# Kernel optimization log

Measured on AMD Instinct MI355X. Metric: run time of the kernel, lower is better.

Reference implementation:

```python
import jax
import jax.numpy as jnp
import numpy as np
from jax import lax

B, T, D = 32, 256, 512   # batch, seq len, controller_dim (== memory_dim)
S = 2048                 # memory_slots
EPS_LN = 1e-5            # nn.LayerNorm default eps
EPS_NRM = 1e-12          # F.normalize default eps


def setup_inputs() -> dict:
    key = jax.random.key(0)
    ks = jax.random.split(key, 12)
    sc = 1.0 / np.sqrt(D)  # roughly torch Linear init scale
    return {
        "controller_seq": jax.random.normal(ks[0], (B, T, D), dtype=jnp.float32),
        "memory": jax.random.normal(ks[1], (S, D), dtype=jnp.float32),
        "Wk": jax.random.normal(ks[2], (D, D), dtype=jnp.float32) * sc,
        "bk": jax.random.normal(ks[3], (D,), dtype=jnp.float32) * sc,
        "We": jax.random.normal(ks[4], (D, D), dtype=jnp.float32) * sc,
        "be": jax.random.normal(ks[5], (D,), dtype=jnp.float32) * sc,
        "Ww": jax.random.normal(ks[6], (D, D), dtype=jnp.float32) * sc,
        "bw": jax.random.normal(ks[7], (D,), dtype=jnp.float32) * sc,
        "Wg": jax.random.normal(ks[8], (D, D), dtype=jnp.float32) * sc,
        "bg": jax.random.normal(ks[9], (D,), dtype=jnp.float32) * sc,
        "gamma": jnp.ones((D,), dtype=jnp.float32),
        "beta": jnp.zeros((D,), dtype=jnp.float32),
    }


def _l2norm(x, axis=-1):
    # matches F.normalize: x / max(||x||, eps)
    n = jnp.sqrt(jnp.sum(x * x, axis=axis, keepdims=True))
    return x / jnp.maximum(n, EPS_NRM)


def _layernorm(x, gamma, beta):
    mu = jnp.mean(x, axis=-1, keepdims=True)
    var = jnp.mean((x - mu) ** 2, axis=-1, keepdims=True)
    return (x - mu) * lax.rsqrt(var + EPS_LN) * gamma + beta


def reference(controller_seq, memory, Wk, bk, We, be, Ww, bw, Wg, bg, gamma, beta):
    batch = controller_seq.shape[0]

    def step(mem, c):  # mem: [S, Dm], c: [B, Dc]
        # --- read (addressing by cosine similarity) ---
        k = c @ Wk.T + bk                       # [B, Dm]
        sim = _l2norm(k) @ _l2norm(mem).T       # [B, S]
        w = jax.nn.softmax(sim, axis=-1)        # [B, S]
        read_val = w @ mem                      # [B, Dm]
        # --- write (erase / add, averaged over batch) ---
        erase = jax.nn.sigmoid(c @ We.T + be)   # [B, Dm]
        add = c @ Ww.T + bw                     # [B, Dm]
        # mean_b (1 - w_bs * e_bd) = 1 - (w^T e)/B ; avoids [B,S,Dm] intermediate
        erase_m = 1.0 - jnp.einsum("bs,bd->sd", w, erase) / batch
        add_m = jnp.einsum("bs,bd->sd", w, add) / batch
        new_mem = _layernorm(mem * erase_m + add_m, gamma, beta)  # dropout in eval mode
        # --- gated output ---
        g = jax.nn.sigmoid(c @ Wg.T + bg)       # [B, Dm]
        out_t = g * c + (1.0 - g) * read_val
        return new_mem, out_t

    _, outs = lax.scan(step, memory, jnp.swapaxes(controller_seq, 0, 1))  # outs: [T, B, D]
    return jnp.swapaxes(outs, 0, 1)  # [B, T, D]
```

## Files before the change

### kernel.cpp

```cpp
#include <hip/hip_runtime.h>

#define DEV __device__ __forceinline__

namespace {
constexpr int Bc = 32;
constexpr int Tc = 256;
constexpr int Dc = 512;
constexpr int Sc = 2048;
constexpr int NBLK = 256;
constexpr int NW   = 128;
constexpr int ROWS = Sc / NW;

constexpr size_t OFF_KN  = 0;
constexpr size_t OFF_E   = OFF_KN  + (size_t)Tc * Bc * Dc;
constexpr size_t OFF_A   = OFF_E   + (size_t)Tc * Bc * Dc;
constexpr size_t OFF_MEM = OFF_A   + (size_t)Tc * Bc * Dc;
constexpr size_t OFF_EW  = OFF_MEM + (size_t)2 * Sc * Dc;
constexpr size_t OFF_RP  = OFF_EW  + (size_t)2 * Sc * Bc;
constexpr size_t OFF_DEN = OFF_RP  + (size_t)2 * 16 * Bc * Dc;
}

DEV float sigm(float x) { return 1.0f / (1.0f + __expf(-x)); }

__global__ __launch_bounds__(256) void k_gemm(
    const float* __restrict__ A,
    const float* __restrict__ Wk, const float* __restrict__ bk,
    const float* __restrict__ We, const float* __restrict__ be,
    const float* __restrict__ Ww, const float* __restrict__ bw,
    const float* __restrict__ Wg, const float* __restrict__ bg,
    float* __restrict__ ws, float* __restrict__ gout)
{
  __shared__ float As[32][68];
  __shared__ float Bs[32][68];

  const int bid = blockIdx.x;
  const int mat = bid >> 10;
  const int rem = bid & 1023;
  const int rt = rem >> 3, jt = rem & 7;
  const int rbase = rt * 64, jbase = jt * 64;

  const float* Wm; const float* bm;
  if      (mat == 0) { Wm = Wk; bm = bk; }
  else if (mat == 1) { Wm = We; bm = be; }
  else if (mat == 2) { Wm = Ww; bm = bw; }
  else               { Wm = Wg; bm = bg; }

  const int tid = threadIdx.x;
  const int lr = tid >> 2;
  const int lk = (tid & 3) * 8;
  const int ty = tid >> 4, tx = tid & 15;

  float acc[4][4] = {};

  for (int k0 = 0; k0 < Dc; k0 += 32) {
    const float4 a0 = *(const float4*)&A [(size_t)(rbase + lr) * Dc + k0 + lk];
    const float4 a1 = *(const float4*)&A [(size_t)(rbase + lr) * Dc + k0 + lk + 4];
    const float4 b0 = *(const float4*)&Wm[(size_t)(jbase + lr) * Dc + k0 + lk];
    const float4 b1 = *(const float4*)&Wm[(size_t)(jbase + lr) * Dc + k0 + lk + 4];
    __syncthreads();
    As[lk + 0][lr] = a0.x; As[lk + 1][lr] = a0.y; As[lk + 2][lr] = a0.z; As[lk + 3][lr] = a0.w;
    As[lk + 4][lr] = a1.x; As[lk + 5][lr] = a1.y; As[lk + 6][lr] = a1.z; As[lk + 7][lr] = a1.w;
    Bs[lk + 0][lr] = b0.x; Bs[lk + 1][lr] = b0.y; Bs[lk + 2][lr] = b0.z; Bs[lk + 3][lr] = b0.w;
    Bs[lk + 4][lr] = b1.x; Bs[lk + 5][lr] = b1.y; Bs[lk + 6][lr] = b1.z; Bs[lk + 7][lr] = b1.w;
    __syncthreads();
    #pragma unroll
    for (int kk = 0; kk < 32; ++kk) {
      const float4 av = *(const float4*)&As[kk][ty * 4];
      const float4 bv = *(const float4*)&Bs[kk][tx * 4];
      const float ar[4] = {av.x, av.y, av.z, av.w};
      const float br[4] = {bv.x, bv.y, bv.z, bv.w};
      #pragma unroll
      for (int i = 0; i < 4; ++i)
        #pragma unroll
        for (int j = 0; j < 4; ++j)
          acc[i][j] = fmaf(ar[i], br[j], acc[i][j]);
    }
  }

  const float4 bias = *(const float4*)&bm[jbase + tx * 4];
  const float bi[4] = {bias.x, bias.y, bias.z, bias.w};
  #pragma unroll
  for (int i = 0; i < 4; ++i) {
    const int r = rbase + ty * 4 + i;
    float v[4];
    #pragma unroll
    for (int j = 0; j < 4; ++j) {
      v[j] = acc[i][j] + bi[j];
      if (mat & 1) v[j] = sigm(v[j]);
    }
    float4 o; o.x = v[0]; o.y = v[1]; o.z = v[2]; o.w = v[3];
    if (mat == 3) {
      *(float4*)&gout[(size_t)r * Dc + jbase + tx * 4] = o;
    } else {
      float* dst = ws + (mat == 0 ? OFF_KN : (mat == 1 ? OFF_E : OFF_A));
      const int t = r & 255, b = r >> 8;
      *(float4*)&dst[((size_t)t * Bc + b) * Dc + jbase + tx * 4] = o;
    }
  }
}

__global__ __launch_bounds__(256) void k_knorm(float* __restrict__ kn)
{
  const int row = blockIdx.x * 4 + (threadIdx.x >> 6);
  const int lane = threadIdx.x & 63;
  float* p = kn + (size_t)row * Dc;
  float4 v0 = *(const float4*)&p[lane * 4];
  float4 v1 = *(const float4*)&p[256 + lane * 4];
  float ss = v0.x*v0.x + v0.y*v0.y + v0.z*v0.z + v0.w*v0.w
           + v1.x*v1.x + v1.y*v1.y + v1.z*v1.z + v1.w*v1.w;
  #pragma unroll
  for (int off = 32; off >= 1; off >>= 1) ss += __shfl_xor(ss, off);
  const float inv = 1.0f / fmaxf(sqrtf(ss), 1e-12f);
  v0.x *= inv; v0.y *= inv; v0.z *= inv; v0.w *= inv;
  v1.x *= inv; v1.y *= inv; v1.z *= inv; v1.w *= inv;
  *(float4*)&p[lane * 4] = v0;
  *(float4*)&p[256 + lane * 4] = v1;
}

DEV void sim_phase(const float* __restrict__ knp, float* __restrict__ ewn,
                   float* __restrict__ denp, float (*xb)[516],
                   const float* invn_s, float* sred, int s0, int tid)
{
  const int r = tid >> 4, bp = tid & 15;
  const float* k0p = knp + (size_t)bp * Dc;
  const float* k1p = knp + (size_t)(bp + 16) * Dc;
  float acc0 = 0.f, acc1 = 0.f;
  #pragma unroll 4
  for (int dq = 0; dq < Dc / 4; ++dq) {
    const float4 y4 = *(const float4*)&xb[r][dq * 4];
    const float4 ka = *(const float4*)&k0p[dq * 4];
    const float4 kb = *(const float4*)&k1p[dq * 4];
    acc0 = fmaf(y4.x, ka.x, acc0); acc0 = fmaf(y4.y, ka.y, acc0);
    acc0 = fmaf(y4.z, ka.z, acc0); acc0 = fmaf(y4.w, ka.w, acc0);
    acc1 = fmaf(y4.x, kb.x, acc1); acc1 = fmaf(y4.y, kb.y, acc1);
    acc1 = fmaf(y4.z, kb.z, acc1); acc1 = fmaf(y4.w, kb.w, acc1);
  }
  const float iv = invn_s[r];
  const float e0 = __expf(acc0 * iv);
  const float e1 = __expf(acc1 * iv);
  ewn[(size_t)(s0 + r) * Bc + bp]      = e0;
  ewn[(size_t)(s0 + r) * Bc + bp + 16] = e1;
  if (tid < 32) sred[tid] = 0.f;
  __syncthreads();
  atomicAdd(&sred[bp], e0);
  atomicAdd(&sred[bp + 16], e1);
  __syncthreads();
  if (tid < 32) atomicAdd(&denp[tid], sred[tid]);
}

__global__ __launch_bounds__(256) void k_prologue(
    const float* __restrict__ mem_in, float* __restrict__ ws)
{
  __shared__ float xbuf[16][516];
  __shared__ float sred[32];
  __shared__ float invn_s[16];

  float* kn   = ws + OFF_KN;
  float* memb = ws + OFF_MEM;
  float* ewb  = ws + OFF_EW;
  float* den  = ws + OFF_DEN;

  const int bid = blockIdx.x, tid = threadIdx.x;
  const int s0 = bid * ROWS;
  const int c0 = tid * 2;
  #pragma unroll
  for (int r = 0; r < ROWS; ++r) {
    const float2 m = *(const float2*)&mem_in[(size_t)(s0 + r) * Dc + c0];
    *(float2*)&xbuf[r][c0] = m;
    *(float2*)&memb[(size_t)(s0 + r) * Dc + c0] = m;
  }
  __syncthreads();
  {
    const int row = tid >> 4, li = tid & 15;
    float ss = 0.f;
    #pragma unroll
    for (int i = 0; i < 8; ++i) {
      const float4 v = *(const float4*)&xbuf[row][(li + i * 16) * 4];
      ss += v.x*v.x + v.y*v.y + v.z*v.z + v.w*v.w;
    }
    ss += __shfl_xor(ss, 8); ss += __shfl_xor(ss, 4);
    ss += __shfl_xor(ss, 2); ss += __shfl_xor(ss, 1);
    if (li == 0) invn_s[row] = 1.0f / fmaxf(sqrtf(ss), 1e-12f);
  }
  __syncthreads();
  sim_phase(kn, ewb, den, xbuf, invn_s, sred, s0, tid);
}

__global__ __launch_bounds__(256) void k_step(
    int t,
    const float* __restrict__ cs,
    const float* __restrict__ gamma, const float* __restrict__ beta,
    float* __restrict__ ws, float* __restrict__ out)
{
  __shared__ float xbuf[16][516];
  __shared__ float wbuf[16][32];
  __shared__ float sred[32];
  __shared__ float mu_s[16], rs_s[16], invn_s[16];
  __shared__ float dinv_s[32];

  float* kn   = ws + OFF_KN;
  float* eptb = ws + OFF_E;
  float* aptb = ws + OFF_A;
  float* memb = ws + OFF_MEM;
  float* ewb  = ws + OFF_EW;
  float* rp   = ws + OFF_RP;
  float* den  = ws + OFF_DEN;

  const int bid = blockIdx.x, tid = threadIdx.x;
  const float inv32 = 1.0f / 32.0f;

  if (bid < NW) {
    if (t < Tc - 1) {
      const int s0 = bid * ROWS;
      const int c0 = tid * 2;
      const float* ewc = ewb + (size_t)(t & 1) * Sc * Bc;
      float*       ewn = ewb + (size_t)((t + 1) & 1) * Sc * Bc;
      const float* memc = memb + (size_t)(t & 1) * Sc * Dc;
      float*       memn = memb + (size_t)((t + 1) & 1) * Sc * Dc;

      if (tid < 32) dinv_s[tid] = 1.0f / den[(size_t)t * Bc + tid];
      __syncthreads();
      for (int idx = tid; idx < ROWS * 32; idx += 256) {
        const int r = idx >> 5, b = idx & 31;
        wbuf[r][b] = ewc[(size_t)(s0 + r) * Bc + b] * dinv_s[b];
      }
      __syncthreads();

      float2 er[ROWS] = {}, ad[ROWS] = {};
      const float* ept = eptb + (size_t)t * Bc * Dc;
      const float* apt = aptb + (size_t)t * Bc * Dc;
      #pragma unroll 4
      for (int b = 0; b < 32; ++b) {
        const float2 ev = *(const float2*)&ept[(size_t)b * Dc + c0];
        const float2 av = *(const float2*)&apt[(size_t)b * Dc + c0];
        #pragma unroll
        for (int r = 0; r < ROWS; ++r) {
          const float wv = wbuf[r][b];
          er[r].x = fmaf(wv, ev.x, er[r].x); er[r].y = fmaf(wv, ev.y, er[r].y);
          ad[r].x = fmaf(wv, av.x, ad[r].x); ad[r].y = fmaf(wv, av.y, ad[r].y);
        }
      }
      float2 xr[ROWS];
      #pragma unroll
      for (int r = 0; r < ROWS; ++r) {
        const float2 m = *(const float2*)&memc[(size_t)(s0 + r) * Dc + c0];
        float2 x;
        x.x = m.x * (1.0f - er[r].x * inv32) + ad[r].x * inv32;
        x.y = m.y * (1.0f - er[r].y * inv32) + ad[r].y * inv32;
        xr[r] = x;
        *(float2*)&xbuf[r][c0] = x;
      }
      __syncthreads();
      {
        const int row = tid >> 4, li = tid & 15;
        float s1 = 0.f, s2 = 0.f;
        #pragma unroll
        for (int i = 0; i < 8; ++i) {
          const float4 v = *(const float4*)&xbuf[row][(li + i * 16) * 4];
          s1 += v.x + v.y + v.z + v.w;
          s2 += v.x*v.x + v.y*v.y + v.z*v.z + v.w*v.w;
        }
        s1 += __shfl_xor(s1, 8); s2 += __shfl_xor(s2, 8);
        s1 += __shfl_xor(s1, 4); s2 += __shfl_xor(s2, 4);
        s1 += __shfl_xor(s1, 2); s2 += __shfl_xor(s2, 2);
        s1 += __shfl_xor(s1, 1); s2 += __shfl_xor(s2, 1);
        if (li == 0) {
          const float mu = s1 * (1.0f / 512.0f);
          const float var = s2 * (1.0f / 512.0f) - mu * mu;
          mu_s[row] = mu;
          rs_s[row] = rsqrtf(var + 1e-5f);
        }
      }
      __syncthreads();
      const float2 gm  = *(const float2*)&gamma[c0];
      const float2 bt2 = *(const float2*)&beta[c0];
      #pragma unroll
      for (int r = 0; r < ROWS; ++r) {
        const float mu = mu_s[r], rs = rs_s[r];
        float2 y;
        y.x = (xr[r].x - mu) * rs * gm.x + bt2.x;
        y.y = (xr[r].y - mu) * rs * gm.y + bt2.y;
        *(float2*)&xbuf[r][c0] = y;
        *(float2*)&memn[(size_t)(s0 + r) * Dc + c0] = y;
      }
      __syncthreads();
      {
        const int row = tid >> 4, li = tid & 15;
        float ss = 0.f;
        #pragma unroll
        for (int i = 0; i < 8; ++i) {
          const float4 v = *(const float4*)&xbuf[row][(li + i * 16) * 4];
          ss += v.x*v.x + v.y*v.y + v.z*v.z + v.w*v.w;
        }
        ss += __shfl_xor(ss, 8); ss += __shfl_xor(ss, 4);
        ss += __shfl_xor(ss, 2); ss += __shfl_xor(ss, 1);
        if (li == 0) invn_s[row] = 1.0f / fmaxf(sqrtf(ss), 1e-12f);
      }
      __syncthreads();
      sim_phase(kn + (size_t)(t + 1) * Bc * Dc, ewn,
                den + (size_t)(t + 1) * Bc, xbuf, invn_s, sred, s0, tid);
    }
  } else {
    const int rb = bid - NW;
    if (rb < 8 && t >= 1) {
      const int t0 = t - 1;
      const float* rpc = rp + (size_t)(t0 & 1) * 16 * Bc * Dc;
      const int base = (rb * 256 + tid) * 8;
      const int b = base >> 9, d0 = base & 511;
      const float inv = 1.0f / den[(size_t)t0 * Bc + b];
      float r0[4] = {}, r1[4] = {};
      #pragma unroll
      for (int si = 0; si < 16; ++si) {
        const float* q = rpc + ((size_t)si * Bc + b) * Dc + d0;
        const float4 p0 = *(const float4*)&q[0];
        const float4 p1 = *(const float4*)&q[4];
        r0[0] += p0.x; r0[1] += p0.y; r0[2] += p0.z; r0[3] += p0.w;
        r1[0] += p1.x; r1[1] += p1.y; r1[2] += p1.z; r1[3] += p1.w;
      }
      const size_t oofs = ((size_t)b * Tc + t0) * Dc + d0;
      const float4 g0 = *(const float4*)&out[oofs];
      const float4 g1 = *(const float4*)&out[oofs + 4];
      const float4 c0v = *(const float4*)&cs[oofs];
      const float4 c1v = *(const float4*)&cs[oofs + 4];
      float4 o0, o1;
      o0.x = g0.x * c0v.x + (1.0f - g0.x) * (r0[0] * inv);
      o0.y = g0.y * c0v.y + (1.0f - g0.y) * (r0[1] * inv);
      o0.z = g0.z * c0v.z + (1.0f - g0.z) * (r0[2] * inv);
      o0.w = g0.w * c0v.w + (1.0f - g0.w) * (r0[3] * inv);
      o1.x = g1.x * c1v.x + (1.0f - g1.x) * (r1[0] * inv);
      o1.y = g1.y * c1v.y + (1.0f - g1.y) * (r1[1] * inv);
      o1.z = g1.z * c1v.z + (1.0f - g1.z) * (r1[2] * inv);
      o1.w = g1.w * c1v.w + (1.0f - g1.w) * (r1[3] * inv);
      *(float4*)&out[oofs] = o0;
      *(float4*)&out[oofs + 4] = o1;
    }
    if (t < Tc) {
      const int si = rb >> 3, dj = rb & 7;
      const int sB = si * 128;
      const float* ewc = ewb + (size_t)(t & 1) * Sc * Bc;
      const float* memc = memb + (size_t)(t & 1) * Sc * Dc;
      float* ewl = (float*)xbuf;
      for (int i = tid; i < 128 * 32; i += 256) ewl[i] = ewc[(size_t)sB * Bc + i];
      __syncthreads();
      const int b = tid >> 3, dg = tid & 7;
      const int cbase = dj * 64 + dg * 8;
      float a0[4] = {}, a1[4] = {};
      #pragma unroll 2
      for (int s = 0; s < 128; ++s) {
        const float wv = ewl[s * 32 + b];
        const float* mrow = memc + (size_t)(sB + s) * Dc + cbase;
        const float4 m0 = *(const float4*)&mrow[0];
        const float4 m1 = *(const float4*)&mrow[4];
        a0[0] = fmaf(wv, m0.x, a0[0]); a0[1] = fmaf(wv, m0.y, a0[1]);
        a0[2] = fmaf(wv, m0.z, a0[2]); a0[3] = fmaf(wv, m0.w, a0[3]);
        a1[0] = fmaf(wv, m1.x, a1[0]); a1[1] = fmaf(wv, m1.y, a1[1]);
        a1[2] = fmaf(wv, m1.z, a1[2]); a1[3] = fmaf(wv, m1.w, a1[3]);
      }
      float* dst = rp + (size_t)(t & 1) * 16 * Bc * Dc + ((size_t)si * Bc + b) * Dc + cbase;
      float4 w0, w1;
      w0.x = a0[0]; w0.y = a0[1]; w0.z = a0[2]; w0.w = a0[3];
      w1.x = a1[0]; w1.y = a1[1]; w1.z = a1[2]; w1.w = a1[3];
      *(float4*)&dst[0] = w0;
      *(float4*)&dst[4] = w1;
    }
  }
}

extern "C" void kernel_launch(void* const* d_in, const int* in_sizes, int n_in,
                              void* d_out, int out_size, void* d_ws, size_t ws_size,
                              hipStream_t stream)
{
  const float* cs    = (const float*)d_in[0];
  const float* mem   = (const float*)d_in[1];
  const float* Wk    = (const float*)d_in[2];
  const float* bk    = (const float*)d_in[3];
  const float* We    = (const float*)d_in[4];
  const float* be    = (const float*)d_in[5];
  const float* Ww    = (const float*)d_in[6];
  const float* bw    = (const float*)d_in[7];
  const float* Wg    = (const float*)d_in[8];
  const float* bg    = (const float*)d_in[9];
  const float* gamma = (const float*)d_in[10];
  const float* beta  = (const float*)d_in[11];
  float* ws  = (float*)d_ws;
  float* out = (float*)d_out;

  hipMemsetAsync(ws + OFF_DEN, 0, (size_t)Tc * Bc * sizeof(float), stream);

  hipLaunchKernelGGL(k_gemm, dim3(4096), dim3(256), 0, stream,
                     cs, Wk, bk, We, be, Ww, bw, Wg, bg, ws, out);
  hipLaunchKernelGGL(k_knorm, dim3(2048), dim3(256), 0, stream, ws + OFF_KN);
  hipLaunchKernelGGL(k_prologue, dim3(NW), dim3(256), 0, stream, mem, ws);

  for (int t = 0; t <= Tc; ++t) {
    hipLaunchKernelGGL(k_step, dim3(NBLK), dim3(256), 0, stream,
                       t, cs, gamma, beta, ws, out);
  }
}
```

Before: 10.78 ms.

## Fuse per-step launches into one persistent kernel with grid barriers

Replaces the 257 per-timestep k_step launches with a single persistent k_main kernel that loops over time and synchronises all 256 blocks through an atomic-counter grid barrier. Cross-block data (memory, exp weights, denominators, partial reads) now goes through relaxed agent-scope atomic loads and stores so it stays visible across blocks inside one launch. This removes per-launch overhead and the kernel-boundary drain, at the cost of spin-waiting, narrower float2 accesses instead of float4, and reliance on all 256 blocks being resident at the same time.

```diff
diff --git a/kernel.cpp b/kernel.cpp
--- a/kernel.cpp
+++ b/kernel.cpp
@@ -18,9 +18,30 @@
 constexpr size_t OFF_EW  = OFF_MEM + (size_t)2 * Sc * Dc;
 constexpr size_t OFF_RP  = OFF_EW  + (size_t)2 * Sc * Bc;
 constexpr size_t OFF_DEN = OFF_RP  + (size_t)2 * 16 * Bc * Dc;
+constexpr size_t OFF_CNT = OFF_DEN + (size_t)Tc * Bc;
 }
 
 DEV float sigm(float x) { return 1.0f / (1.0f + __expf(-x)); }
+
+DEV float ld1cg(const float* p) {
+  unsigned u = __hip_atomic_load((const unsigned*)p, __ATOMIC_RELAXED,
+                                 __HIP_MEMORY_SCOPE_AGENT);
+  return __uint_as_float(u);
+}
+DEV void st1cg(float* p, float v) {
+  __hip_atomic_store((unsigned*)p, __float_as_uint(v), __ATOMIC_RELAXED,
+                     __HIP_MEMORY_SCOPE_AGENT);
+}
+DEV float2 ld2cg(const float* p) {
+  unsigned long long u = __hip_atomic_load((const unsigned long long*)p,
+                                           __ATOMIC_RELAXED, __HIP_MEMORY_SCOPE_AGENT);
+  union { unsigned long long u; float2 f; } c; c.u = u; return c.f;
+}
+DEV void st2cg(float* p, float2 v) {
+  union { float2 f; unsigned long long u; } c; c.f = v;
+  __hip_atomic_store((unsigned long long*)p, c.u, __ATOMIC_RELAXED,
+                     __HIP_MEMORY_SCOPE_AGENT);
+}
 
 __global__ __launch_bounds__(256) void k_gemm(
     const float* __restrict__ A,
@@ -138,8 +159,8 @@
   const float iv = invn_s[r];
   const float e0 = __expf(acc0 * iv);
   const float e1 = __expf(acc1 * iv);
-  ewn[(size_t)(s0 + r) * Bc + bp]      = e0;
-  ewn[(size_t)(s0 + r) * Bc + bp + 16] = e1;
+  st1cg(&ewn[(size_t)(s0 + r) * Bc + bp], e0);
+  st1cg(&ewn[(size_t)(s0 + r) * Bc + bp + 16], e1);
   if (tid < 32) sred[tid] = 0.f;
   __syncthreads();
   atomicAdd(&sred[bp], e0);
@@ -167,7 +188,7 @@
   for (int r = 0; r < ROWS; ++r) {
     const float2 m = *(const float2*)&mem_in[(size_t)(s0 + r) * Dc + c0];
     *(float2*)&xbuf[r][c0] = m;
-    *(float2*)&memb[(size_t)(s0 + r) * Dc + c0] = m;
+    st2cg(&memb[(size_t)(s0 + r) * Dc + c0], m);
   }
   __syncthreads();
   {
@@ -186,8 +207,21 @@
   sim_phase(kn, ewb, den, xbuf, invn_s, sred, s0, tid);
 }
 
-__global__ __launch_bounds__(256) void k_step(
-    int t,
+DEV void gbar(unsigned* cnt, unsigned target)
+{
+  __syncthreads();
+  if (threadIdx.x == 0) {
+    __hip_atomic_fetch_add(cnt, 1u, __ATOMIC_RELAXED, __HIP_MEMORY_SCOPE_AGENT);
+    unsigned v = __hip_atomic_load(cnt, __ATOMIC_RELAXED, __HIP_MEMORY_SCOPE_AGENT);
+    while (v < target) {
+      __builtin_amdgcn_s_sleep(2);
+      v = __hip_atomic_load(cnt, __ATOMIC_RELAXED, __HIP_MEMORY_SCOPE_AGENT);
+    }
+  }
+  __syncthreads();
+}
+
+__global__ __launch_bounds__(256) void k_main(
     const float* __restrict__ cs,
     const float* __restrict__ gamma, const float* __restrict__ beta,
     float* __restrict__ ws, float* __restrict__ out)
@@ -205,164 +239,174 @@
   float* ewb  = ws + OFF_EW;
   float* rp   = ws + OFF_RP;
   float* den  = ws + OFF_DEN;
+  unsigned* cnt = (unsigned*)(ws + OFF_CNT);
 
   const int bid = blockIdx.x, tid = threadIdx.x;
   const float inv32 = 1.0f / 32.0f;
-
-  if (bid < NW) {
-    if (t < Tc - 1) {
-      const int s0 = bid * ROWS;
-      const int c0 = tid * 2;
-      const float* ewc = ewb + (size_t)(t & 1) * Sc * Bc;
-      float*       ewn = ewb + (size_t)((t + 1) & 1) * Sc * Bc;
-      const float* memc = memb + (size_t)(t & 1) * Sc * Dc;
-      float*       memn = memb + (size_t)((t + 1) & 1) * Sc * Dc;
-
-      if (tid < 32) dinv_s[tid] = 1.0f / den[(size_t)t * Bc + tid];
-      __syncthreads();
-      for (int idx = tid; idx < ROWS * 32; idx += 256) {
-        const int r = idx >> 5, b = idx & 31;
-        wbuf[r][b] = ewc[(size_t)(s0 + r) * Bc + b] * dinv_s[b];
-      }
-      __syncthreads();
-
-      float2 er[ROWS] = {}, ad[ROWS] = {};
-      const float* ept = eptb + (size_t)t * Bc * Dc;
-      const float* apt = aptb + (size_t)t * Bc * Dc;
-      #pragma unroll 4
-      for (int b = 0; b < 32; ++b) {
-        const float2 ev = *(const float2*)&ept[(size_t)b * Dc + c0];
-        const float2 av = *(const float2*)&apt[(size_t)b * Dc + c0];
+  unsigned bart = 0;
+
+  for (int t = 0; t <= Tc; ++t) {
+    if (bid < NW) {
+      if (t < Tc - 1) {
+        const int s0 = bid * ROWS;
+        const int c0 = tid * 2;
+        const float* ewc = ewb + (size_t)(t & 1) * Sc * Bc;
+        float*       ewn = ewb + (size_t)((t + 1) & 1) * Sc * Bc;
+        const float* memc = memb + (size_t)(t & 1) * Sc * Dc;
+        float*       memn = memb + (size_t)((t + 1) & 1) * Sc * Dc;
+
+        if (tid < 32) dinv_s[tid] = 1.0f / ld1cg(&den[(size_t)t * Bc + tid]);
+        __syncthreads();
+        for (int idx = tid; idx < ROWS * 32; idx += 256) {
+          const int r = idx >> 5, b = idx & 31;
+          wbuf[r][b] = ld1cg(&ewc[(size_t)(s0 + r) * Bc + b]) * dinv_s[b];
+        }
+        __syncthreads();
+
+        float2 er[ROWS] = {}, ad[ROWS] = {};
+        const float* ept = eptb + (size_t)t * Bc * Dc;
+        const float* apt = aptb + (size_t)t * Bc * Dc;
+        #pragma unroll 4
+        for (int b = 0; b < 32; ++b) {
+          const float2 ev = *(const float2*)&ept[(size_t)b * Dc + c0];
+          const float2 av = *(const float2*)&apt[(size_t)b * Dc + c0];
+          #pragma unroll
+          for (int r = 0; r < ROWS; ++r) {
+            const float wv = wbuf[r][b];
+            er[r].x = fmaf(wv, ev.x, er[r].x); er[r].y = fmaf(wv, ev.y, er[r].y);
+            ad[r].x = fmaf(wv, av.x, ad[r].x); ad[r].y = fmaf(wv, av.y, ad[r].y);
+          }
+        }
+        float2 xr[ROWS];
         #pragma unroll
         for (int r = 0; r < ROWS; ++r) {
-          const float wv = wbuf[r][b];
-          er[r].x = fmaf(wv, ev.x, er[r].x); er[r].y = fmaf(wv, ev.y, er[r].y);
-          ad[r].x = fmaf(wv, av.x, ad[r].x); ad[r].y = fmaf(wv, av.y, ad[r].y);
-        }
+          const float2 m = ld2cg(&memc[(size_t)(s0 + r) * Dc + c0]);
+          float2 x;
+          x.x = m.x * (1.0f - er[r].x * inv32) + ad[r].x * inv32;
+          x.y = m.y * (1.0f - er[r].y * inv32) + ad[r].y * inv32;
+          xr[r] = x;
+          *(float2*)&xbuf[r][c0] = x;
+        }
+        __syncthreads();
+        {
+          const int row = tid >> 4, li = tid & 15;
+          float s1 = 0.f, s2 = 0.f;
+          #pragma unroll
+          for (int i = 0; i < 8; ++i) {
+            const float4 v = *(const float4*)&xbuf[row][(li + i * 16) * 4];
+            s1 += v.x + v.y + v.z + v.w;
+            s2 += v.x*v.x + v.y*v.y + v.z*v.z + v.w*v.w;
+          }
+          s1 += __shfl_xor(s1, 8); s2 += __shfl_xor(s2, 8);
+          s1 += __shfl_xor(s1, 4); s2 += __shfl_xor(s2, 4);
+          s1 += __shfl_xor(s1, 2); s2 += __shfl_xor(s2, 2);
+          s1 += __shfl_xor(s1, 1); s2 += __shfl_xor(s2, 1);
+          if (li == 0) {
+            const float mu = s1 * (1.0f / 512.0f);
+            const float var = s2 * (1.0f / 512.0f) - mu * mu;
+            mu_s[row] = mu;
+            rs_s[row] = rsqrtf(var + 1e-5f);
+          }
+        }
+        __syncthreads();
+        const float2 gm  = *(const float2*)&gamma[c0];
+        const float2 bt2 = *(const float2*)&beta[c0];
+        #pragma unroll
+        for (int r = 0; r < ROWS; ++r) {
+          const float mu = mu_s[r], rs = rs_s[r];
+          float2 y;
+          y.x = (xr[r].x - mu) * rs * gm.x + bt2.x;
+          y.y = (xr[r].y - mu) * rs * gm.y + bt2.y;
+          *(float2*)&xbuf[r][c0] = y;
+          st2cg(&memn[(size_t)(s0 + r) * Dc + c0], y);
+        }
+        __syncthreads();
+        {
+          const int row = tid >> 4, li = tid & 15;
+          float ss = 0.f;
+          #pragma unroll
+          for (int i = 0; i < 8; ++i) {
+            const float4 v = *(const float4*)&xbuf[row][(li + i * 16) * 4];
+            ss += v.x*v.x + v.y*v.y + v.z*v.z + v.w*v.w;
+          }
+          ss += __shfl_xor(ss, 8); ss += __shfl_xor(ss, 4);
+          ss += __shfl_xor(ss, 2); ss += __shfl_xor(ss, 1);
+          if (li == 0) invn_s[row] = 1.0f / fmaxf(sqrtf(ss), 1e-12f);
+        }
+        __syncthreads();
+        sim_phase(kn + (size_t)(t + 1) * Bc * Dc, ewn,
+                  den + (size_t)(t + 1) * Bc, xbuf, invn_s, sred, s0, tid);
       }
-      float2 xr[ROWS];
-      #pragma unroll
-      for (int r = 0; r < ROWS; ++r) {
-        const float2 m = *(const float2*)&memc[(size_t)(s0 + r) * Dc + c0];
-        float2 x;
-        x.x = m.x * (1.0f - er[r].x * inv32) + ad[r].x * inv32;
-        x.y = m.y * (1.0f - er[r].y * inv32) + ad[r].y * inv32;
-        xr[r] = x;
-        *(float2*)&xbuf[r][c0] = x;
+    } else {
+      const int rb = bid - NW;
+      if (rb < 8 && t >= 1) {
+        const int t0 = t - 1;
+        const float* rpc = rp + (size_t)(t0 & 1) * 16 * Bc * Dc;
+        const int base = (rb * 256 + tid) * 8;
+        const int b = base >> 9, d0 = base & 511;
+        const float inv = 1.0f / ld1cg(&den[(size_t)t0 * Bc + b]);
+        float r0[8] = {};
+        #pragma unroll
+        for (int si = 0; si < 16; ++si) {
+          const float* q = rpc + ((size_t)si * Bc + b) * Dc + d0;
+          const float2 p0 = ld2cg(q + 0);
+          const float2 p1 = ld2cg(q + 2);
+          const float2 p2 = ld2cg(q + 4);
+          const float2 p3 = ld2cg(q + 6);
+          r0[0] += p0.x; r0[1] += p0.y; r0[2] += p1.x; r0[3] += p1.y;
+          r0[4] += p2.x; r0[5] += p2.y; r0[6] += p3.x; r0[7] += p3.y;
+        }
+        const size_t oofs = ((size_t)b * Tc + t0) * Dc + d0;
+        const float4 g0 = *(const float4*)&out[oofs];
+        const float4 g1 = *(const float4*)&out[oofs + 4];
+        const float4 c0v = *(const float4*)&cs[oofs];
+        const float4 c1v = *(const float4*)&cs[oofs + 4];
+        float4 o0, o1;
+        o0.x = g0.x * c0v.x + (1.0f - g0.x) * (r0[0] * inv);
+        o0.y = g0.y * c0v.y + (1.0f - g0.y) * (r0[1] * inv);
+        o0.z = g0.z * c0v.z + (1.0f - g0.z) * (r0[2] * inv);
+        o0.w = g0.w * c0v.w + (1.0f - g0.w) * (r0[3] * inv);
+        o1.x = g1.x * c1v.x + (1.0f - g1.x) * (r0[4] * inv);
+        o1.y = g1.y * c1v.y + (1.0f - g1.y) * (r0[5] * inv);
+        o1.z = g1.z * c1v.z + (1.0f - g1.z) * (r0[6] * inv);
+        o1.w = g1.w * c1v.w + (1.0f - g1.w) * (r0[7] * inv);
+        *(float4*)&out[oofs] = o0;
+        *(float4*)&out[oofs + 4] = o1;
       }
-      __syncthreads();
-      {
-        const int row = tid >> 4, li = tid & 15;
-        float s1 = 0.f, s2 = 0.f;
-        #pragma unroll
-        for (int i = 0; i < 8; ++i) {
-          const float4 v = *(const float4*)&xbuf[row][(li + i * 16) * 4];
-          s1 += v.x + v.y + v.z + v.w;
-          s2 += v.x*v.x + v.y*v.y + v.z*v.z + v.w*v.w;
-        }
-        s1 += __shfl_xor(s1, 8); s2 += __shfl_xor(s2, 8);
-        s1 += __shfl_xor(s1, 4); s2 += __shfl_xor(s2, 4);
-        s1 += __shfl_xor(s1, 2); s2 += __shfl_xor(s2, 2);
-        s1 += __shfl_xor(s1, 1); s2 += __shfl_xor(s2, 1);
-        if (li == 0) {
-          const float mu = s1 * (1.0f / 512.0f);
-          const float var = s2 * (1.0f / 512.0f) - mu * mu;
-          mu_s[row] = mu;
-          rs_s[row] = rsqrtf(var + 1e-5f);
-        }
+      if (t < Tc) {
+        const int si = rb >> 3, dj = rb & 7;
+        const int sB = si * 128;
+        const float* ewc = ewb + (size_t)(t & 1) * Sc * Bc;
+        const float* memc = memb + (size_t)(t & 1) * Sc * Dc;
+        float* ewl = (float*)xbuf;
+        for (int i = tid; i < 128 * 32; i += 256)
+          ewl[i] = ld1cg(&ewc[(size_t)sB * Bc + i]);
+        __syncthreads();
+        const int b = tid >> 3, dg = tid & 7;
+        const int cbase = dj * 64 + dg * 8;
+        float a0[8] = {};
+        #pragma unroll 2
+        for (int s = 0; s < 128; ++s) {
+          const float wv = ewl[s * 32 + b];
+          const float* mrow = memc + (size_t)(sB + s) * Dc + cbase;
+          const float2 m0 = ld2cg(mrow + 0);
+          const float2 m1 = ld2cg(mrow + 2);
+          const float2 m2 = ld2cg(mrow + 4);
+          const float2 m3 = ld2cg(mrow + 6);
+          a0[0] = fmaf(wv, m0.x, a0[0]); a0[1] = fmaf(wv, m0.y, a0[1]);
+          a0[2] = fmaf(wv, m1.x, a0[2]); a0[3] = fmaf(wv, m1.y, a0[3]);
+          a0[4] = fmaf(wv, m2.x, a0[4]); a0[5] = fmaf(wv, m2.y, a0[5]);
+          a0[6] = fmaf(wv, m3.x, a0[6]); a0[7] = fmaf(wv, m3.y, a0[7]);
+        }
+        float* dst = rp + (size_t)(t & 1) * 16 * Bc * Dc + ((size_t)si * Bc + b) * Dc + cbase;
+        float2 w0; w0.x = a0[0]; w0.y = a0[1]; st2cg(dst + 0, w0);
+        float2 w1; w1.x = a0[2]; w1.y = a0[3]; st2cg(dst + 2, w1);
+        float2 w2; w2.x = a0[4]; w2.y = a0[5]; st2cg(dst + 4, w2);
+        float2 w3; w3.x = a0[6]; w3.y = a0[7]; st2cg(dst + 6, w3);
+        __syncthreads();
       }
-      __syncthreads();
-      const float2 gm  = *(const float2*)&gamma[c0];
-      const float2 bt2 = *(const float2*)&beta[c0];
-      #pragma unroll
-      for (int r = 0; r < ROWS; ++r) {
-        const float mu = mu_s[r], rs = rs_s[r];
-        float2 y;
-        y.x = (xr[r].x - mu) * rs * gm.x + bt2.x;
-        y.y = (xr[r].y - mu) * rs * gm.y + bt2.y;
-        *(float2*)&xbuf[r][c0] = y;
-        *(float2*)&memn[(size_t)(s0 + r) * Dc + c0] = y;
-      }
-      __syncthreads();
-      {
-        const int row = tid >> 4, li = tid & 15;
-        float ss = 0.f;
-        #pragma unroll
-        for (int i = 0; i < 8; ++i) {
-          const float4 v = *(const float4*)&xbuf[row][(li + i * 16) * 4];
-          ss += v.x*v.x + v.y*v.y + v.z*v.z + v.w*v.w;
-        }
-        ss += __shfl_xor(ss, 8); ss += __shfl_xor(ss, 4);
-        ss += __shfl_xor(ss, 2); ss += __shfl_xor(ss, 1);
-        if (li == 0) invn_s[row] = 1.0f / fmaxf(sqrtf(ss), 1e-12f);
-      }
-      __syncthreads();
-      sim_phase(kn + (size_t)(t + 1) * Bc * Dc, ewn,
-                den + (size_t)(t + 1) * Bc, xbuf, invn_s, sred, s0, tid);
-    }
-  } else {
-    const int rb = bid - NW;
-    if (rb < 8 && t >= 1) {
-      const int t0 = t - 1;
-      const float* rpc = rp + (size_t)(t0 & 1) * 16 * Bc * Dc;
-      const int base = (rb * 256 + tid) * 8;
-      const int b = base >> 9, d0 = base & 511;
-      const float inv = 1.0f / den[(size_t)t0 * Bc + b];
-      float r0[4] = {}, r1[4] = {};
-      #pragma unroll
-      for (int si = 0; si < 16; ++si) {
-        const float* q = rpc + ((size_t)si * Bc + b) * Dc + d0;
-        const float4 p0 = *(const float4*)&q[0];
-        const float4 p1 = *(const float4*)&q[4];
-        r0[0] += p0.x; r0[1] += p0.y; r0[2] += p0.z; r0[3] += p0.w;
-        r1[0] += p1.x; r1[1] += p1.y; r1[2] += p1.z; r1[3] += p1.w;
-      }
-      const size_t oofs = ((size_t)b * Tc + t0) * Dc + d0;
-      const float4 g0 = *(const float4*)&out[oofs];
-      const float4 g1 = *(const float4*)&out[oofs + 4];
-      const float4 c0v = *(const float4*)&cs[oofs];
-      const float4 c1v = *(const float4*)&cs[oofs + 4];
-      float4 o0, o1;
-      o0.x = g0.x * c0v.x + (1.0f - g0.x) * (r0[0] * inv);
-      o0.y = g0.y * c0v.y + (1.0f - g0.y) * (r0[1] * inv);
-      o0.z = g0.z * c0v.z + (1.0f - g0.z) * (r0[2] * inv);
-      o0.w = g0.w * c0v.w + (1.0f - g0.w) * (r0[3] * inv);
-      o1.x = g1.x * c1v.x + (1.0f - g1.x) * (r1[0] * inv);
-      o1.y = g1.y * c1v.y + (1.0f - g1.y) * (r1[1] * inv);
-      o1.z = g1.z * c1v.z + (1.0f - g1.z) * (r1[2] * inv);
-      o1.w = g1.w * c1v.w + (1.0f - g1.w) * (r1[3] * inv);
-      *(float4*)&out[oofs] = o0;
-      *(float4*)&out[oofs + 4] = o1;
-    }
-    if (t < Tc) {
-      const int si = rb >> 3, dj = rb & 7;
-      const int sB = si * 128;
-      const float* ewc = ewb + (size_t)(t & 1) * Sc * Bc;
-      const float* memc = memb + (size_t)(t & 1) * Sc * Dc;
-      float* ewl = (float*)xbuf;
-      for (int i = tid; i < 128 * 32; i += 256) ewl[i] = ewc[(size_t)sB * Bc + i];
-      __syncthreads();
-      const int b = tid >> 3, dg = tid & 7;
-      const int cbase = dj * 64 + dg * 8;
-      float a0[4] = {}, a1[4] = {};
-      #pragma unroll 2
-      for (int s = 0; s < 128; ++s) {
-        const float wv = ewl[s * 32 + b];
-        const float* mrow = memc + (size_t)(sB + s) * Dc + cbase;
-        const float4 m0 = *(const float4*)&mrow[0];
-        const float4 m1 = *(const float4*)&mrow[4];
-        a0[0] = fmaf(wv, m0.x, a0[0]); a0[1] = fmaf(wv, m0.y, a0[1]);
-        a0[2] = fmaf(wv, m0.z, a0[2]); a0[3] = fmaf(wv, m0.w, a0[3]);
-        a1[0] = fmaf(wv, m1.x, a1[0]); a1[1] = fmaf(wv, m1.y, a1[1]);
-        a1[2] = fmaf(wv, m1.z, a1[2]); a1[3] = fmaf(wv, m1.w, a1[3]);
-      }
-      float* dst = rp + (size_t)(t & 1) * 16 * Bc * Dc + ((size_t)si * Bc + b) * Dc + cbase;
-      float4 w0, w1;
-      w0.x = a0[0]; w0.y = a0[1]; w0.z = a0[2]; w0.w = a0[3];
-      w1.x = a1[0]; w1.y = a1[1]; w1.z = a1[2]; w1.w = a1[3];
-      *(float4*)&dst[0] = w0;
-      *(float4*)&dst[4] = w1;
-    }
+    }
+    if (t < Tc) { bart += NBLK; gbar(cnt, bart); }
   }
 }
 
@@ -385,15 +429,12 @@
   float* ws  = (float*)d_ws;
   float* out = (float*)d_out;
 
-  hipMemsetAsync(ws + OFF_DEN, 0, (size_t)Tc * Bc * sizeof(float), stream);
+  hipMemsetAsync(ws + OFF_DEN, 0, ((size_t)Tc * Bc + 1) * sizeof(float), stream);
 
   hipLaunchKernelGGL(k_gemm, dim3(4096), dim3(256), 0, stream,
                      cs, Wk, bk, We, be, Ww, bw, Wg, bg, ws, out);
   hipLaunchKernelGGL(k_knorm, dim3(2048), dim3(256), 0, stream, ws + OFF_KN);
   hipLaunchKernelGGL(k_prologue, dim3(NW), dim3(256), 0, stream, mem, ws);
-
-  for (int t = 0; t <= Tc; ++t) {
-    hipLaunchKernelGGL(k_step, dim3(NBLK), dim3(256), 0, stream,
-                       t, cs, gamma, beta, ws, out);
-  }
-}
+  hipLaunchKernelGGL(k_main, dim3(NBLK), dim3(256), 0, stream,
+                     cs, gamma, beta, ws, out);
+}
```

Measured after the change: 12.15 ms. 1.13x slower.
